# Kernel optimization log

Hardware: AMD Instinct MI355X
Metric: run time of the kernel (lower is better)

Reference implementation:

```python
import jax, jax.numpy as jnp
import numpy as np

B = 64; FEAT = 16; T = 32001; BANDS = 8; ND = 16
OUT_LEN = 32000; N_TAPS = 43; K_LATE = 1024
FLIP_PROB = 0.1  # 1 - stickiness (0.9)


def _dense(k, fan_in, fan_out, scale=1.0):
    return jax.random.normal(k, (fan_in, fan_out), jnp.float32) * (scale / np.sqrt(fan_in))


def setup_inputs() -> dict:
    key = jax.random.key(0)
    ks = jax.random.split(key, 20)
    z32 = lambda n: jnp.zeros((n,), jnp.float32)
    inp = {}
    inp['x'] = jax.random.normal(ks[0], (B, FEAT), jnp.float32)
    # stand-in LSTM decoder params: (B, FEAT) -> (B, T, BANDS)
    inp['lstm_W1'] = _dense(ks[1], FEAT, 64); inp['lstm_b1'] = z32(64)
    inp['lstm_W2'] = _dense(ks[2], 64, T * BANDS); inp['lstm_b2'] = z32(T * BANDS)
    # EDCToFDNMapper params
    inp['enc_W1'] = _dense(ks[3], 2 * BANDS, 64); inp['enc_b1'] = z32(64)
    inp['enc_W2'] = _dense(ks[4], 64, 64); inp['enc_b2'] = z32(64)
    inp['del_W1'] = _dense(ks[5], 3 + 64, 64); inp['del_b1'] = z32(64)
    inp['del_W2'] = _dense(ks[6], 64, ND); inp['del_b2'] = z32(ND)
    inp['alp_W1'] = _dense(ks[7], 64, 32); inp['alp_b1'] = z32(32)
    inp['alp_W2'] = _dense(ks[8], 32, ND); inp['alp_b2'] = z32(ND)
    inp['bet_W1'] = _dense(ks[9], 64, 32); inp['bet_b1'] = z32(32)
    inp['bet_W2'] = _dense(ks[10], 32, ND); inp['bet_b2'] = z32(ND)
    # EarlyReflections gains (nn.Parameter, zeros-init in torch; random here to exercise math)
    inp['early_gains'] = jax.random.normal(ks[11], (N_TAPS,), jnp.float32) * 0.1
    # DifferentiableFDN surrogate: causal decaying FIR reverb kernel
    decay = jnp.exp(-jnp.arange(K_LATE, dtype=jnp.float32) / 256.0)
    inp['late_kernel'] = jax.random.normal(ks[12], (K_LATE,), jnp.float32) * 0.05 * decay
    # sticky-sign flip events (constant random draws, flip prob = 1 - stickiness)
    inp['flips'] = (jax.random.uniform(ks[13], (B, OUT_LEN)) < FLIP_PROB).astype(jnp.int32)
    return inp


def _causal_conv(sig, gains):
    # torch: F.conv1d(x[:,None,:], gains.flip(0)[None,None,:], padding=K-1)[:, 0, :L]
    # (torch conv1d is correlation; flipping makes it true convolution with gains)
    K = gains.shape[0]
    y = jax.lax.conv_general_dilated(sig[:, None, :], gains[::-1][None, None, :], (1,),
                                     [(K - 1, K - 1)], dimension_numbers=('NCH', 'OIH', 'NCH'))
    return y[:, 0, :sig.shape[1]]


def _mlp2(h, W1, b1, W2, b2):  # Linear-ReLU-Linear
    return jax.nn.relu(h @ W1 + b1) @ W2 + b2


def reference(x, lstm_W1, lstm_b1, lstm_W2, lstm_b2,
              enc_W1, enc_b1, enc_W2, enc_b2,
              del_W1, del_b1, del_W2, del_b2,
              alp_W1, alp_b1, alp_W2, alp_b2,
              bet_W1, bet_b1, bet_W2, bet_b2,
              early_gains, late_kernel, flips):
    Bx = x.shape[0]
    # LSTM stand-in: (B, FEAT) -> (B, T, BANDS)
    edc_pred = _mlp2(x, lstm_W1, lstm_b1, lstm_W2, lstm_b2).reshape(Bx, T, BANDS)
    edc_1d = edc_pred.mean(axis=2)  # (B, T)
    # EDCToFDNMapper
    edc_mean = edc_pred.mean(axis=1)
    q1 = edc_pred[:, :T // 4, :].mean(axis=1)
    q4 = edc_pred[:, 3 * T // 4:, :].mean(axis=1)
    edc_feat = jnp.concatenate([edc_mean, q4 - q1], axis=1)  # (B, 2*BANDS)
    h = jax.nn.relu(_mlp2(edc_feat, enc_W1, enc_b1, enc_W2, enc_b2))  # Linear-ReLU-Linear-ReLU
    delay_in = jnp.concatenate([x[:, :3], h], axis=1)
    log_kappa = _mlp2(delay_in, del_W1, del_b1, del_W2, del_b2)
    alpha_raw = _mlp2(h, alp_W1, alp_b1, alp_W2, alp_b2)
    beta_raw = _mlp2(h, bet_W1, bet_b1, bet_W2, bet_b2)
    # late reverb (FDN surrogate) + early reflections, both causal convs on edc_1d
    late = _causal_conv(edc_1d, late_kernel)[:, :OUT_LEN]   # (B, 32000)
    early = _causal_conv(edc_1d, early_gains)[:, :OUT_LEN]  # (B, 32000)
    # sign-sticky phase reconstruction: signs = (-1)^cumsum(flips[:,1:]) (parallel parity scan)
    diff = edc_1d[:, :-1] - edc_1d[:, 1:]
    amp = jnp.sqrt(jnp.clip(diff, 0.0))  # (B, T-1) == (B, 32000)
    par = jnp.cumsum(flips.at[:, 0].set(0), axis=1) % 2  # loop starts at t=1; signs[:,0]=+1
    phase = amp * (1.0 - 2.0 * par.astype(amp.dtype))
    rir = (early + late) * phase
    return (rir, edc_pred, log_kappa, alpha_raw, beta_raw)
```

## Files before the change

### kernel.cpp

```cpp
#include <hip/hip_runtime.h>
#include <hip/hip_bf16.h>

#define LJ 256008
#define TN 32001
#define OUT_LEN 32000

typedef __attribute__((ext_vector_type(8))) short short8v;
typedef __attribute__((ext_vector_type(8))) __bf16 bf16x8;
typedef __attribute__((ext_vector_type(4))) float f32x4;

__device__ __forceinline__ unsigned short f2bu(float f) {
    union { __hip_bfloat16 h; unsigned short u; } cv; cv.h = __float2bfloat16(f); return cv.u;
}
__device__ __forceinline__ uint4 pack8(const unsigned short* h) {
    return make_uint4((unsigned)h[0] | ((unsigned)h[1] << 16),
                      (unsigned)h[2] | ((unsigned)h[3] << 16),
                      (unsigned)h[4] | ((unsigned)h[5] << 16),
                      (unsigned)h[6] | ((unsigned)h[7] << 16));
}
__device__ __forceinline__ f32x4 mfma16(uint4 a, uint4 b, f32x4 c) {
    union { uint4 u; short8v s; bf16x8 v; } ua, ub;
    ua.u = a; ub.u = b;
    return __builtin_amdgcn_mfma_f32_16x16x32_bf16(ua.v, ub.v, c, 0, 0, 0);
}

__global__ __launch_bounds__(256) void k_h1(const float* __restrict__ x,
                                            const float* __restrict__ W1,
                                            const float* __restrict__ b1,
                                            float* __restrict__ h1)
{
    int idx = blockIdx.x * 256 + threadIdx.x;
    if (idx >= 4096) return;
    int b = idx >> 6, i = idx & 63;
    float acc = b1[i];
    #pragma unroll
    for (int f = 0; f < 16; ++f)
        acc += x[b * 16 + f] * W1[f * 64 + i];
    h1[i * 64 + b] = fmaxf(acc, 0.f);
}

__global__ __launch_bounds__(512) void k_gemm(const float* __restrict__ W2,
                                              const float* __restrict__ b2,
                                              const float* __restrict__ h1,
                                              float* __restrict__ edc,
                                              float* __restrict__ edc1d,
                                              float* __restrict__ P)
{
    __shared__ float h1f[4096];
    __shared__ float w2f[8192];
    __shared__ __align__(16) unsigned short afr[4096];
    __shared__ float wband[2048];
    __shared__ float bband[32];
    int tid = threadIdx.x;
    long C0 = (long)blockIdx.x * 256;
    float4 z4 = make_float4(0.f, 0.f, 0.f, 0.f);

    #pragma unroll
    for (int s = 0; s < 8; ++s) h1f[tid + 512 * s] = h1[tid + 512 * s];
    {
        int bt = tid >> 7, kb = (tid >> 6) & 1, l = tid & 63;
        int q = l >> 4, r = l & 15;
        unsigned short hh[8];
        #pragma unroll
        for (int e = 0; e < 8; ++e)
            hh[e] = f2bu(h1[(32 * kb + 8 * q + e) * 64 + 16 * bt + r]);
        *(uint4*)(&afr[tid * 8]) = pack8(hh);
    }
    if (tid < 32) {
        long c8 = C0 + 8 * tid;
        float sum = 0.f;
        if (c8 + 7 < LJ) {
            float4 u0 = *(const float4*)(b2 + c8);
            float4 u1 = *(const float4*)(b2 + c8 + 4);
            sum = ((u0.x + u0.y) + (u0.z + u0.w)) + ((u1.x + u1.y) + (u1.z + u1.w));
        }
        bband[tid] = sum;
    }
    #pragma unroll
    for (int s = 0; s < 4; ++s) {
        int slot = tid + 512 * s;
        int row = slot >> 6, c4 = slot & 63;
        long col = C0 + 4 * c4;
        float4 v = (col < LJ) ? *(const float4*)(W2 + (long)row * LJ + col) : z4;
        *(float4*)(&w2f[row * 256 + 4 * c4]) = v;
    }
    __syncthreads();

    int lane = tid & 63, wv = tid >> 6;
    int q = lane >> 4, r = lane & 15;
    f32x4 acc[2][4];
    #pragma unroll
    for (int c = 0; c < 2; ++c)
        #pragma unroll
        for (int b = 0; b < 4; ++b) acc[c][b] = (f32x4){0.f, 0.f, 0.f, 0.f};

    #pragma unroll
    for (int s = 0; s < 2; ++s) {
        int en = tid + 512 * s;
        int i = en >> 5, tl = en & 31;
        const float* p = &w2f[i * 256 + 8 * tl];
        wband[i * 32 + tl] = ((p[0] + p[1]) + (p[2] + p[3])) + ((p[4] + p[5]) + (p[6] + p[7]));
    }
    #pragma unroll
    for (int ctl = 0; ctl < 2; ++ctl) {
        int ct = wv * 2 + ctl;
        unsigned short hh[8];
        #pragma unroll
        for (int e = 0; e < 8; ++e)
            hh[e] = f2bu(w2f[(8 * q + e) * 256 + 16 * ct + r]);
        uint4 braw = pack8(hh);
        #pragma unroll
        for (int bt = 0; bt < 4; ++bt) {
            uint4 araw = *(const uint4*)(&afr[((bt * 2 + 0) * 64 + lane) * 8]);
            acc[ctl][bt] = mfma16(araw, braw, acc[ctl][bt]);
        }
    }
    __syncthreads();
    #pragma unroll
    for (int s = 0; s < 4; ++s) {
        int slot = tid + 512 * s;
        int row = slot >> 6, c4 = slot & 63;
        long col = C0 + 4 * c4;
        float4 v = (col < LJ) ? *(const float4*)(W2 + (long)(32 + row) * LJ + col) : z4;
        *(float4*)(&w2f[row * 256 + 4 * c4]) = v;
    }
    __syncthreads();
    #pragma unroll
    for (int s = 0; s < 2; ++s) {
        int en = tid + 512 * s;
        int i2 = en >> 5, tl = en & 31;
        const float* p = &w2f[i2 * 256 + 8 * tl];
        wband[(32 + i2) * 32 + tl] = ((p[0] + p[1]) + (p[2] + p[3])) + ((p[4] + p[5]) + (p[6] + p[7]));
    }
    #pragma unroll
    for (int ctl = 0; ctl < 2; ++ctl) {
        int ct = wv * 2 + ctl;
        unsigned short hh[8];
        #pragma unroll
        for (int e = 0; e < 8; ++e)
            hh[e] = f2bu(w2f[(8 * q + e) * 256 + 16 * ct + r]);
        uint4 braw = pack8(hh);
        #pragma unroll
        for (int bt = 0; bt < 4; ++bt) {
            uint4 araw = *(const uint4*)(&afr[((bt * 2 + 1) * 64 + lane) * 8]);
            acc[ctl][bt] = mfma16(araw, braw, acc[ctl][bt]);
        }
    }
    __syncthreads();

    #pragma unroll
    for (int s = 0; s < 4; ++s) {
        int en = tid + 512 * s;
        int b = en >> 5, tl = en & 31;
        long c8 = C0 + 8 * tl;
        if (c8 + 7 < LJ) {
            float dot = bband[tl];
            #pragma unroll 8
            for (int i = 0; i < 64; ++i)
                dot += h1f[i * 64 + b] * wband[i * 32 + tl];
            edc1d[(long)b * TN + (C0 >> 3) + tl] = dot * 0.125f;
        }
    }

    float psum[4][4];
    #pragma unroll
    for (int bt = 0; bt < 4; ++bt)
        #pragma unroll
        for (int rg = 0; rg < 4; ++rg) psum[bt][rg] = 0.f;
    #pragma unroll
    for (int ctl = 0; ctl < 2; ++ctl) {
        int ct = wv * 2 + ctl;
        long col = C0 + 16 * ct + r;
        bool okc = col < LJ;
        float bias = okc ? b2[col] : 0.f;
        #pragma unroll
        for (int bt = 0; bt < 4; ++bt) {
            #pragma unroll
            for (int rg = 0; rg < 4; ++rg) {
                float v = acc[ctl][bt][rg] + bias;
                if (okc) edc[(long)(16 * bt + 4 * q + rg) * LJ + col] = v;
                float sps = v + __shfl_xor(v, 8);
                psum[bt][rg] += sps;
            }
        }
    }
    if (r < 8) {
        #pragma unroll
        for (int bt = 0; bt < 4; ++bt)
            #pragma unroll
            for (int rg = 0; rg < 4; ++rg)
                P[(long)blockIdx.x * 512 + (16 * bt + 4 * q + rg) * 8 + r] = psum[bt][rg];
    }
}

__global__ __launch_bounds__(512) void k_redsum(const float* __restrict__ P,
                                                float* __restrict__ sums)
{
    int g = blockIdx.x, t = threadIdx.x;
    int b = t >> 3, band = t & 7;
    int s0 = g * 16, s1 = s0 + 16;
    if (s1 > 1001) s1 = 1001;
    float all = 0.f, q1 = 0.f, q4 = 0.f;
    for (int blk = s0; blk < s1; ++blk) {
        float v = P[(long)blk * 512 + t];
        all += v;
        if (blk < 250) q1 += v;
        if (blk >= 750) q4 += v;
    }
    atomicAdd(&sums[b * 24 + band * 3 + 0], all);
    atomicAdd(&sums[b * 24 + band * 3 + 1], q1);
    atomicAdd(&sums[b * 24 + band * 3 + 2], q4);
}

__global__ __launch_bounds__(64) void k_mlp(const float* __restrict__ x,
    const float* __restrict__ sums,
    const float* __restrict__ eW1, const float* __restrict__ eb1,
    const float* __restrict__ eW2, const float* __restrict__ eb2,
    const float* __restrict__ dW1, const float* __restrict__ db1,
    const float* __restrict__ dW2, const float* __restrict__ db2,
    const float* __restrict__ aW1, const float* __restrict__ ab1,
    const float* __restrict__ aW2, const float* __restrict__ ab2,
    const float* __restrict__ bW1, const float* __restrict__ bb1,
    const float* __restrict__ bW2, const float* __restrict__ bb2,
    float* __restrict__ out_lk, float* __restrict__ out_a, float* __restrict__ out_b)
{
    int b = blockIdx.x, o = threadIdx.x;
    __shared__ float feat[16], a1[64], hh[64], t1[64];
    if (o < 16) {
        float v;
        if (o < 8) v = sums[b * 24 + o * 3] * (1.f / 32001.f);
        else {
            int band = o - 8;
            v = sums[b * 24 + band * 3 + 2] * (1.f / 8001.f)
              - sums[b * 24 + band * 3 + 1] * (1.f / 8000.f);
        }
        feat[o] = v;
    }
    __syncthreads();
    {   float acc = eb1[o];
        #pragma unroll
        for (int c = 0; c < 16; ++c) acc += feat[c] * eW1[c * 64 + o];
        a1[o] = fmaxf(acc, 0.f); }
    __syncthreads();
    {   float acc = eb2[o];
        for (int c = 0; c < 64; ++c) acc += a1[c] * eW2[c * 64 + o];
        hh[o] = fmaxf(acc, 0.f); }
    __syncthreads();
    {   float acc = db1[o];
        #pragma unroll
        for (int c = 0; c < 3; ++c) acc += x[b * 16 + c] * dW1[c * 64 + o];
        for (int c = 0; c < 64; ++c) acc += hh[c] * dW1[(3 + c) * 64 + o];
        t1[o] = fmaxf(acc, 0.f); }
    __syncthreads();
    if (o < 16) {
        float acc = db2[o];
        for (int c = 0; c < 64; ++c) acc += t1[c] * dW2[c * 16 + o];
        out_lk[b * 16 + o] = acc;
    }
    __syncthreads();
    if (o < 32) {
        float acc = ab1[o];
        for (int c = 0; c < 64; ++c) acc += hh[c] * aW1[c * 32 + o];
        t1[o] = fmaxf(acc, 0.f);
    }
    __syncthreads();
    if (o < 16) {
        float acc = ab2[o];
        for (int c = 0; c < 32; ++c) acc += t1[c] * aW2[c * 16 + o];
        out_a[b * 16 + o] = acc;
    }
    __syncthreads();
    if (o < 32) {
        float acc = bb1[o];
        for (int c = 0; c < 64; ++c) acc += hh[c] * bW1[c * 32 + o];
        t1[o] = fmaxf(acc, 0.f);
    }
    __syncthreads();
    if (o < 16) {
        float acc = bb2[o];
        for (int c = 0; c < 32; ++c) acc += t1[c] * bW2[c * 16 + o];
        out_b[b * 16 + o] = acc;
    }
}

__global__ __launch_bounds__(256) void k_par1(const int* __restrict__ flips,
                                              unsigned* __restrict__ parbits,
                                              unsigned* __restrict__ ctot)
{
    int b = blockIdx.x, c = blockIdx.y, tid = threadIdx.x;
    int t = c * 256 + tid;
    int bit = (t == 0) ? 0 : (flips[(long)b * OUT_LEN + t] & 1);
    int lane = tid & 63, wv = tid >> 6;
    unsigned long long mask = __ballot(bit != 0);
    int below = ((int)__popcll(mask & ((1ull << lane) - 1ull))) & 1;
    int incl = below ^ bit;
    __shared__ int wtot[4];
    if (lane == 0) wtot[wv] = ((int)__popcll(mask)) & 1;
    __syncthreads();
    int pre = 0;
    for (int w = 0; w < wv; ++w) pre ^= wtot[w];
    int inclB = pre ^ incl;
    unsigned long long m2 = __ballot(inclB != 0);
    if (lane == 0)  parbits[b * 1000 + c * 8 + wv * 2 + 0] = (unsigned)(m2 & 0xffffffffull);
    if (lane == 32) parbits[b * 1000 + c * 8 + wv * 2 + 1] = (unsigned)(m2 >> 32);
    if (tid == 0) ctot[c * 64 + b] = (unsigned)(wtot[0] ^ wtot[1] ^ wtot[2] ^ wtot[3]);
}

__global__ __launch_bounds__(64) void k_par2(const unsigned* __restrict__ ctot,
                                             unsigned* __restrict__ cpref)
{
    int b = threadIdx.x;
    unsigned carry = 0;
    for (int c = 0; c < 125; ++c) {
        cpref[c * 64 + b] = carry;
        carry ^= ctot[c * 64 + b];
    }
}

__global__ __launch_bounds__(512) void k_convm(const float* __restrict__ edc1d,
    const float* __restrict__ lk, const float* __restrict__ eg,
    const unsigned* __restrict__ parbits, const unsigned* __restrict__ cpref,
    float* __restrict__ rir)
{
    __shared__ float kerf[1024];
    __shared__ __align__(16) unsigned short afr[33 * 64 * 8];
    __shared__ __align__(16) unsigned short sbf[3136];
    __shared__ float sf32[2049];
    int b = blockIdx.x, tb0 = blockIdx.y * 2048, tid = threadIdx.x;
    const float* src = edc1d + (long)b * TN;
    for (int k = tid; k < 1024; k += 512)
        kerf[k] = lk[k] + (k < 43 ? eg[k] : 0.f);
    for (int ch = tid; ch < 388; ch += 512) {
        unsigned short h[8];
        #pragma unroll
        for (int e = 0; e < 8; ++e) {
            int gt = tb0 + ch * 8 + e - 1031;
            float v = (gt >= 0 && gt <= OUT_LEN) ? src[gt] : 0.f;
            h[e] = f2bu(v);
        }
        int cs = ch ^ ((ch >> 3) & 7);
        *(uint4*)(&sbf[cs * 8]) = pack8(h);
    }
    for (int u = tid; u < 2049; u += 512) {
        int gt = tb0 + u;
        sf32[u] = (gt <= OUT_LEN) ? src[gt] : 0.f;
    }
    __syncthreads();
    for (int sl = tid; sl < 33 * 64; sl += 512) {
        int kb = sl >> 6, l = sl & 63;
        int x0 = kb * 32 - 1 + (l & 15) - 8 * (l >> 4);
        unsigned short h[8];
        #pragma unroll
        for (int e = 0; e < 8; ++e) {
            int x = x0 - e;
            float v = (x >= 0 && x < 1024) ? kerf[x] : 0.f;
            h[e] = f2bu(v);
        }
        *(uint4*)(&afr[sl * 8]) = pack8(h);
    }
    __syncthreads();
    int lane = tid & 63, wv = tid >> 6;
    int tb = tb0 + wv * 256;
    int cq = wv * 256 + 16 * (lane & 15) + 8 * (lane >> 4) + 1032;
    f32x4 acc = {0.f, 0.f, 0.f, 0.f};
    for (int kb = 0; kb < 33; ++kb) {
        uint4 araw = *(const uint4*)(&afr[(kb * 64 + lane) * 8]);
        int ch = (cq - (kb << 5)) >> 3;
        int cs = ch ^ ((ch >> 3) & 7);
        uint4 braw = *(const uint4*)(&sbf[cs * 8]);
        acc = mfma16(araw, braw, acc);
    }
    int c = lane & 15, q = lane >> 4;
    int t4 = tb + 16 * c + 4 * q;
    if (t4 < OUT_LEN) {
        int u0 = t4 - tb0;
        unsigned pw = parbits[b * 1000 + (t4 >> 5)];
        unsigned cp = cpref[(t4 >> 8) * 64 + b] & 1u;
        int sh = t4 & 31;
        float sv[5];
        #pragma unroll
        for (int e = 0; e < 5; ++e) sv[e] = sf32[u0 + e];
        float r[4];
        #pragma unroll
        for (int reg = 0; reg < 4; ++reg) {
            float diff = sv[reg] - sv[reg + 1];
            float amp = diff > 0.f ? sqrtf(diff) : 0.f;
            unsigned p = ((pw >> (sh + reg)) & 1u) ^ cp;
            r[reg] = acc[reg] * amp * (p ? -1.f : 1.f);
        }
        *(float4*)(rir + (long)b * OUT_LEN + t4) = make_float4(r[0], r[1], r[2], r[3]);
    }
}

extern "C" void kernel_launch(void* const* d_in, const int* in_sizes, int n_in,
                              void* d_out, int out_size, void* d_ws, size_t ws_size,
                              hipStream_t stream) {
    (void)in_sizes; (void)n_in; (void)out_size; (void)ws_size;
    const float* x    = (const float*)d_in[0];
    const float* lW1  = (const float*)d_in[1];  const float* lb1 = (const float*)d_in[2];
    const float* lW2  = (const float*)d_in[3];  const float* lb2 = (const float*)d_in[4];
    const float* eW1  = (const float*)d_in[5];  const float* eb1 = (const float*)d_in[6];
    const float* eW2  = (const float*)d_in[7];  const float* eb2 = (const float*)d_in[8];
    const float* dW1  = (const float*)d_in[9];  const float* db1 = (const float*)d_in[10];
    const float* dW2  = (const float*)d_in[11]; const float* db2 = (const float*)d_in[12];
    const float* aW1  = (const float*)d_in[13]; const float* ab1 = (const float*)d_in[14];
    const float* aW2  = (const float*)d_in[15]; const float* ab2 = (const float*)d_in[16];
    const float* bW1  = (const float*)d_in[17]; const float* bb1 = (const float*)d_in[18];
    const float* bW2  = (const float*)d_in[19]; const float* bb2 = (const float*)d_in[20];
    const float* eg   = (const float*)d_in[21]; const float* lkk = (const float*)d_in[22];
    const int* flips  = (const int*)d_in[23];

    float* out = (float*)d_out;
    float* rir = out;
    float* edc = out + 2048000;
    float* olk = out + 18432512;
    float* oa  = out + 18433536;
    float* ob  = out + 18434560;

    char* wsb = (char*)d_ws;
    float*    ws_h1   = (float*)(wsb + 1024);
    unsigned* ws_ct   = (unsigned*)(wsb + 18432);
    unsigned* ws_cp   = (unsigned*)(wsb + 50688);
    unsigned* ws_pb   = (unsigned*)(wsb + 82944);
    float*    ws_sums = (float*)(wsb + 339200);
    float*    ws_e1d  = (float*)(wsb + 346112);
    float*    ws_part = (float*)(wsb + 8538368);

    hipMemsetAsync(ws_sums, 0, 64 * 24 * sizeof(float), stream);

    k_h1<<<16, 256, 0, stream>>>(x, lW1, lb1, ws_h1);
    k_par1<<<dim3(64, 125), 256, 0, stream>>>(flips, ws_pb, ws_ct);
    k_par2<<<1, 64, 0, stream>>>(ws_ct, ws_cp);
    k_gemm<<<1001, 512, 0, stream>>>(lW2, lb2, ws_h1, edc, ws_e1d, ws_part);
    k_redsum<<<63, 512, 0, stream>>>(ws_part, ws_sums);
    k_mlp<<<64, 64, 0, stream>>>(x, ws_sums, eW1, eb1, eW2, eb2, dW1, db1, dW2, db2,
                                 aW1, ab1, aW2, ab2, bW1, bb1, bW2, bb2, olk, oa, ob);
    k_convm<<<dim3(64, 16), 512, 0, stream>>>(ws_e1d, lkk, eg, ws_pb, ws_cp, rir);
}
```

Baseline: 101.3 us.

## Split band-mean and EDC statistics out of GEMM using linearity over W2

The band-averaged edc_1d computation and the per-batch partial sums move out of the main GEMM kernel into a separate kernel, k_e1d, which re-reads W2 and computes both from column sums of W2. Statistics are then formed algebraically as h1 times summed weights, plus the bias sums, in a single-block k_sums kernel. This replaces the k_redsum kernel and the memset. The GEMM loses its h1 shared copy, its extra reductions and its shuffles, which should shrink LDS use and epilogue work. In exchange, W2 (about 65 MB) is read a second time and an extra launch is added, and k_sums is a serial single-block reduction over 1001 partials.

```diff
diff --git a/kernel.cpp b/kernel.cpp
--- a/kernel.cpp
+++ b/kernel.cpp
@@ -42,21 +42,14 @@
 __global__ __launch_bounds__(512) void k_gemm(const float* __restrict__ W2,
                                               const float* __restrict__ b2,
                                               const float* __restrict__ h1,
-                                              float* __restrict__ edc,
-                                              float* __restrict__ edc1d,
-                                              float* __restrict__ P)
-{
-    __shared__ float h1f[4096];
+                                              float* __restrict__ edc)
+{
     __shared__ float w2f[8192];
     __shared__ __align__(16) unsigned short afr[4096];
-    __shared__ float wband[2048];
-    __shared__ float bband[32];
     int tid = threadIdx.x;
     long C0 = (long)blockIdx.x * 256;
     float4 z4 = make_float4(0.f, 0.f, 0.f, 0.f);
 
-    #pragma unroll
-    for (int s = 0; s < 8; ++s) h1f[tid + 512 * s] = h1[tid + 512 * s];
     {
         int bt = tid >> 7, kb = (tid >> 6) & 1, l = tid & 63;
         int q = l >> 4, r = l & 15;
@@ -65,16 +58,6 @@
         for (int e = 0; e < 8; ++e)
             hh[e] = f2bu(h1[(32 * kb + 8 * q + e) * 64 + 16 * bt + r]);
         *(uint4*)(&afr[tid * 8]) = pack8(hh);
-    }
-    if (tid < 32) {
-        long c8 = C0 + 8 * tid;
-        float sum = 0.f;
-        if (c8 + 7 < LJ) {
-            float4 u0 = *(const float4*)(b2 + c8);
-            float4 u1 = *(const float4*)(b2 + c8 + 4);
-            sum = ((u0.x + u0.y) + (u0.z + u0.w)) + ((u1.x + u1.y) + (u1.z + u1.w));
-        }
-        bband[tid] = sum;
     }
     #pragma unroll
     for (int s = 0; s < 4; ++s) {
@@ -95,13 +78,6 @@
         for (int b = 0; b < 4; ++b) acc[c][b] = (f32x4){0.f, 0.f, 0.f, 0.f};
 
     #pragma unroll
-    for (int s = 0; s < 2; ++s) {
-        int en = tid + 512 * s;
-        int i = en >> 5, tl = en & 31;
-        const float* p = &w2f[i * 256 + 8 * tl];
-        wband[i * 32 + tl] = ((p[0] + p[1]) + (p[2] + p[3])) + ((p[4] + p[5]) + (p[6] + p[7]));
-    }
-    #pragma unroll
     for (int ctl = 0; ctl < 2; ++ctl) {
         int ct = wv * 2 + ctl;
         unsigned short hh[8];
@@ -126,13 +102,6 @@
     }
     __syncthreads();
     #pragma unroll
-    for (int s = 0; s < 2; ++s) {
-        int en = tid + 512 * s;
-        int i2 = en >> 5, tl = en & 31;
-        const float* p = &w2f[i2 * 256 + 8 * tl];
-        wband[(32 + i2) * 32 + tl] = ((p[0] + p[1]) + (p[2] + p[3])) + ((p[4] + p[5]) + (p[6] + p[7]));
-    }
-    #pragma unroll
     for (int ctl = 0; ctl < 2; ++ctl) {
         int ct = wv * 2 + ctl;
         unsigned short hh[8];
@@ -146,70 +115,147 @@
             acc[ctl][bt] = mfma16(araw, braw, acc[ctl][bt]);
         }
     }
-    __syncthreads();
-
-    #pragma unroll
-    for (int s = 0; s < 4; ++s) {
-        int en = tid + 512 * s;
-        int b = en >> 5, tl = en & 31;
-        long c8 = C0 + 8 * tl;
-        if (c8 + 7 < LJ) {
-            float dot = bband[tl];
-            #pragma unroll 8
-            for (int i = 0; i < 64; ++i)
-                dot += h1f[i * 64 + b] * wband[i * 32 + tl];
-            edc1d[(long)b * TN + (C0 >> 3) + tl] = dot * 0.125f;
-        }
-    }
-
-    float psum[4][4];
-    #pragma unroll
-    for (int bt = 0; bt < 4; ++bt)
-        #pragma unroll
-        for (int rg = 0; rg < 4; ++rg) psum[bt][rg] = 0.f;
+
     #pragma unroll
     for (int ctl = 0; ctl < 2; ++ctl) {
         int ct = wv * 2 + ctl;
         long col = C0 + 16 * ct + r;
-        bool okc = col < LJ;
-        float bias = okc ? b2[col] : 0.f;
-        #pragma unroll
-        for (int bt = 0; bt < 4; ++bt) {
+        if (col < LJ) {
+            float bias = b2[col];
             #pragma unroll
-            for (int rg = 0; rg < 4; ++rg) {
-                float v = acc[ctl][bt][rg] + bias;
-                if (okc) edc[(long)(16 * bt + 4 * q + rg) * LJ + col] = v;
-                float sps = v + __shfl_xor(v, 8);
-                psum[bt][rg] += sps;
+            for (int bt = 0; bt < 4; ++bt)
+                #pragma unroll
+                for (int rg = 0; rg < 4; ++rg)
+                    edc[(long)(16 * bt + 4 * q + rg) * LJ + col] = acc[ctl][bt][rg] + bias;
+        }
+    }
+}
+
+__global__ __launch_bounds__(256) void k_e1d(const float* __restrict__ W2,
+                                             const float* __restrict__ b2,
+                                             const float* __restrict__ h1,
+                                             float* __restrict__ edc1d,
+                                             float* __restrict__ wbP)
+{
+    __shared__ float h1T[64 * 68];
+    __shared__ float wbndT[32 * 68];
+    int tid = threadIdx.x;
+    long C0 = (long)blockIdx.x * 256;
+
+    #pragma unroll
+    for (int s = 0; s < 16; ++s) {
+        int g = tid + 256 * s;
+        h1T[(g & 63) * 68 + (g >> 6)] = h1[g];
+    }
+    #pragma unroll
+    for (int s = 0; s < 8; ++s) {
+        int e = tid + 256 * s;
+        int i = e >> 5, tl = e & 31;
+        long c8 = C0 + 8 * tl;
+        float v0 = 0.f, v1 = 0.f, v2 = 0.f, v3 = 0.f, v4 = 0.f, v5 = 0.f, v6 = 0.f, v7 = 0.f;
+        if (c8 + 7 < LJ) {
+            float4 u0 = *(const float4*)(W2 + (long)i * LJ + c8);
+            float4 u1 = *(const float4*)(W2 + (long)i * LJ + c8 + 4);
+            v0 = u0.x; v1 = u0.y; v2 = u0.z; v3 = u0.w;
+            v4 = u1.x; v5 = u1.y; v6 = u1.z; v7 = u1.w;
+        }
+        wbndT[tl * 68 + i] = ((v0 + v1) + (v2 + v3)) + ((v4 + v5) + (v6 + v7));
+        float bv[8] = {v0, v1, v2, v3, v4, v5, v6, v7};
+        #pragma unroll
+        for (int m = 1; m < 32; m <<= 1)
+            #pragma unroll
+            for (int bd = 0; bd < 8; ++bd)
+                bv[bd] += __shfl_xor(bv[bd], m);
+        if (tl == 0) {
+            #pragma unroll
+            for (int bd = 0; bd < 8; ++bd)
+                wbP[(long)blockIdx.x * 512 + i * 8 + bd] = bv[bd];
+        }
+    }
+    __syncthreads();
+
+    int tl = tid & 31;
+    int b0 = tid >> 5;
+    long c8 = C0 + 8 * tl;
+    if (c8 + 7 < LJ) {
+        float4 bb0 = *(const float4*)(b2 + c8);
+        float4 bb1 = *(const float4*)(b2 + c8 + 4);
+        float bias = ((bb0.x + bb0.y) + (bb0.z + bb0.w)) + ((bb1.x + bb1.y) + (bb1.z + bb1.w));
+        float d[8];
+        #pragma unroll
+        for (int k = 0; k < 8; ++k) d[k] = bias;
+        #pragma unroll
+        for (int i0 = 0; i0 < 64; i0 += 4) {
+            float4 wA = *(const float4*)(&wbndT[tl * 68 + i0]);
+            #pragma unroll
+            for (int k = 0; k < 8; ++k) {
+                float4 hA = *(const float4*)(&h1T[(b0 + 8 * k) * 68 + i0]);
+                d[k] += hA.x * wA.x + hA.y * wA.y + hA.z * wA.z + hA.w * wA.w;
             }
         }
-    }
-    if (r < 8) {
-        #pragma unroll
-        for (int bt = 0; bt < 4; ++bt)
+        int tcol = (int)(C0 >> 3) + tl;
+        #pragma unroll
+        for (int k = 0; k < 8; ++k)
+            edc1d[(long)(b0 + 8 * k) * TN + tcol] = d[k] * 0.125f;
+    }
+}
+
+__global__ __launch_bounds__(512) void k_sums(const float* __restrict__ wbP,
+                                              const float* __restrict__ b2,
+                                              const float* __restrict__ h1,
+                                              float* __restrict__ sums)
+{
+    __shared__ float wbL[512], wbL1[512], wbL4[512];
+    __shared__ float bsum[24];
+    int tid = threadIdx.x;
+    {
+        float all = 0.f, q1 = 0.f, q4 = 0.f;
+        for (int blk = 0; blk < 1001; ++blk) {
+            float v = wbP[(long)blk * 512 + tid];
+            all += v;
+            if (blk < 250) q1 += v;
+            if (blk >= 750) q4 += v;
+        }
+        wbL[tid] = all; wbL1[tid] = q1; wbL4[tid] = q4;
+    }
+    if (tid < 24) bsum[tid] = 0.f;
+    __syncthreads();
+    {
+        float a[8] = {0,0,0,0,0,0,0,0}, s1[8] = {0,0,0,0,0,0,0,0}, s4[8] = {0,0,0,0,0,0,0,0};
+        for (int t = tid; t <= 32000; t += 512) {
+            float4 u0 = *(const float4*)(b2 + 8 * t);
+            float4 u1 = *(const float4*)(b2 + 8 * t + 4);
+            float vv[8] = {u0.x, u0.y, u0.z, u0.w, u1.x, u1.y, u1.z, u1.w};
             #pragma unroll
-            for (int rg = 0; rg < 4; ++rg)
-                P[(long)blockIdx.x * 512 + (16 * bt + 4 * q + rg) * 8 + r] = psum[bt][rg];
-    }
-}
-
-__global__ __launch_bounds__(512) void k_redsum(const float* __restrict__ P,
-                                                float* __restrict__ sums)
-{
-    int g = blockIdx.x, t = threadIdx.x;
-    int b = t >> 3, band = t & 7;
-    int s0 = g * 16, s1 = s0 + 16;
-    if (s1 > 1001) s1 = 1001;
-    float all = 0.f, q1 = 0.f, q4 = 0.f;
-    for (int blk = s0; blk < s1; ++blk) {
-        float v = P[(long)blk * 512 + t];
-        all += v;
-        if (blk < 250) q1 += v;
-        if (blk >= 750) q4 += v;
-    }
-    atomicAdd(&sums[b * 24 + band * 3 + 0], all);
-    atomicAdd(&sums[b * 24 + band * 3 + 1], q1);
-    atomicAdd(&sums[b * 24 + band * 3 + 2], q4);
+            for (int bd = 0; bd < 8; ++bd) {
+                a[bd] += vv[bd];
+                if (t < 8000) s1[bd] += vv[bd];
+                if (t >= 24000) s4[bd] += vv[bd];
+            }
+        }
+        #pragma unroll
+        for (int bd = 0; bd < 8; ++bd) {
+            atomicAdd(&bsum[bd * 3 + 0], a[bd]);
+            atomicAdd(&bsum[bd * 3 + 1], s1[bd]);
+            atomicAdd(&bsum[bd * 3 + 2], s4[bd]);
+        }
+    }
+    __syncthreads();
+    {
+        int b = tid >> 3, band = tid & 7;
+        float accA = bsum[band * 3 + 0];
+        float acc1 = bsum[band * 3 + 1];
+        float acc4 = bsum[band * 3 + 2];
+        for (int i = 0; i < 64; ++i) {
+            float h = h1[i * 64 + b];
+            accA += h * wbL[i * 8 + band];
+            acc1 += h * wbL1[i * 8 + band];
+            acc4 += h * wbL4[i * 8 + band];
+        }
+        sums[b * 24 + band * 3 + 0] = accA;
+        sums[b * 24 + band * 3 + 1] = acc1;
+        sums[b * 24 + band * 3 + 2] = acc4;
+    }
 }
 
 __global__ __launch_bounds__(64) void k_mlp(const float* __restrict__ x,
@@ -424,15 +470,14 @@
     unsigned* ws_pb   = (unsigned*)(wsb + 82944);
     float*    ws_sums = (float*)(wsb + 339200);
     float*    ws_e1d  = (float*)(wsb + 346112);
-    float*    ws_part = (float*)(wsb + 8538368);
-
-    hipMemsetAsync(ws_sums, 0, 64 * 24 * sizeof(float), stream);
+    float*    ws_wbp  = (float*)(wsb + 8538368);
 
     k_h1<<<16, 256, 0, stream>>>(x, lW1, lb1, ws_h1);
     k_par1<<<dim3(64, 125), 256, 0, stream>>>(flips, ws_pb, ws_ct);
     k_par2<<<1, 64, 0, stream>>>(ws_ct, ws_cp);
-    k_gemm<<<1001, 512, 0, stream>>>(lW2, lb2, ws_h1, edc, ws_e1d, ws_part);
-    k_redsum<<<63, 512, 0, stream>>>(ws_part, ws_sums);
+    k_gemm<<<1001, 512, 0, stream>>>(lW2, lb2, ws_h1, edc);
+    k_e1d<<<1001, 256, 0, stream>>>(lW2, lb2, ws_h1, ws_e1d, ws_wbp);
+    k_sums<<<1, 512, 0, stream>>>(ws_wbp, lb2, ws_h1, ws_sums);
     k_mlp<<<64, 64, 0, stream>>>(x, ws_sums, eW1, eb1, eW2, eb2, dW1, db1, dW2, db2,
                                  aW1, ab1, aW2, ab2, bW1, bb1, bW2, bb2, olk, oa, ob);
     k_convm<<<dim3(64, 16), 512, 0, stream>>>(ws_e1d, lkk, eg, ws_pb, ws_cp, rir);
```

Result: slower. 227.4 us (+124.6%).
